# Kernel tuning notes

Hardware: AMD Instinct MI355X
Metric: run time of the kernel (lower is better)

The kernel has to match this reference:

```python
import jax, jax.numpy as jnp
import numpy as np

P = 2
SZ = 224
NIMG = 4
LX, LY, LF, LO = 32, 32, 3, 3
PL, PR, PT, PB = 16, 15, 16, 15
PFO = 1
NFREQ, NORIENT, NPHASE = 12, 8, 2
NFEAT = NPHASE * NORIENT * NFREQ  # 192
CX = SZ + PT + PB - LY + 1  # 224
CY = SZ + PL + PR - LX + 1  # 224


def _gauss(l, w):
    t = np.linspace(-1.0, 1.0, l)
    g = 1.0 / (np.sqrt(2.0 * np.pi) * w) * np.exp(-t ** 2 / (2.0 * w ** 2))
    return g.astype(np.float32)


def _conv2d(x, k):
    # x: [N,1,H,W], k: [1,1,kh,kw]; VALID cross-correlation, matching F.conv2d
    return jax.lax.conv_general_dilated(
        x, k, window_strides=(1, 1), padding='VALID',
        dimension_numbers=('NCHW', 'OIHW', 'NCHW'))


def setup_inputs() -> dict:
    key = jax.random.key(0)
    x = jax.random.normal(key, (NIMG, NFEAT, SZ, SZ), dtype=jnp.float32)
    return {"x": x}


def reference(x):
    gx = jnp.asarray(_gauss(LX, 1.0)).reshape(1, 1, 1, LX)
    gy = jnpy = jnp.asarray(_gauss(LY, 1.0)).reshape(1, 1, LY, 1)
    gf = jnp.asarray(_gauss(LF, 1.0)).reshape(1, 1, LF, 1)
    go = jnp.asarray(_gauss(LO, 1.0)).reshape(1, 1, 1, LO)

    x_p = x ** P
    x_p = jnp.pad(x_p, ((0, 0), (0, 0), (PT, PB), (PL, PR)))  # [B,192,255,255]
    # permute to [feat, img, H, W] then flatten features*imgs into batch
    t = jnp.transpose(x_p, (1, 0, 2, 3)).reshape(NFEAT * NIMG, 1, SZ + PT + PB, SZ + PL + PR)
    t = _conv2d(t, gx)  # [feat*img,1,255,224]
    t = _conv2d(t, gy)  # [feat*img,1,224,224]
    t = t.reshape(NFREQ, NORIENT, NPHASE, NIMG, 1, CX, CY)
    # -> [CX, CY, phase, img, 1, freq, orient]
    t = jnp.transpose(t, (5, 6, 2, 3, 4, 0, 1)).reshape(-1, 1, NFREQ, NORIENT)
    t = jnp.pad(t, ((0, 0), (0, 0), (PFO, PFO), (PFO, PFO)))  # [M,1,14,10]
    t = _conv2d(t, gf)  # [M,1,12,10]
    t = _conv2d(t, go)  # [M,1,12,8]
    B = t.reshape(CX, CY, NPHASE, NIMG, NFREQ, NORIENT)
    return jnp.transpose(B, (3, 4, 5, 2, 0, 1))  # [img,freq,orient,phase,CX,CY]
```

## Files before the change

kernel.cpp:

```cpp
#include <hip/hip_runtime.h>
#include <hip/hip_fp16.h>
#include <math.h>


#define SZW   224
#define PLANE (224*224)
#define PW    256

struct GaussArgs {
    float wx[32];
    float w30;
    float w31;
};

__device__ __forceinline__ int swz(int g) { return g ^ ((g >> 3) & 7); }

__global__ __launch_bounds__(512, 6) void pass1_kernel(const float* __restrict__ in,
                                                       __half* __restrict__ ws,
                                                       const GaussArgs ga)
{
    __shared__ float s2[48 * PW];

    const int tid   = threadIdx.x;
    const int y     = blockIdx.x;
    const int by    = blockIdx.y;
    const int phase = by & 1;
    const int fg    = by >> 1;
    const int img   = blockIdx.z;

    const float w31 = ga.w31;
    const float w30 = ga.w30;

    if (tid < 384) {
        const int lf  = tid >> 6;
        const int xp4 = tid & 63;
        const int f   = 4*fg - 1 + lf;
        const int gsw = swz(xp4);
        float4 a[8];
        if (f >= 0 && f < 12 && xp4 >= 4 && xp4 < 60) {
            const int x0 = xp4*4 - 16;
            const float* base = in + (size_t)(img*192 + f*16 + phase)*PLANE + y*SZW + x0;
            #pragma unroll
            for (int o = 0; o < 8; ++o) {
                float4 v = *reinterpret_cast<const float4*>(base + o*2*PLANE);
                a[o] = make_float4(v.x*v.x, v.y*v.y, v.z*v.z, v.w*v.w);
            }
        } else {
            #pragma unroll
            for (int o = 0; o < 8; ++o) a[o] = make_float4(0.f,0.f,0.f,0.f);
        }
        #pragma unroll
        for (int o = 0; o < 8; ++o) {
            float4 l = (o > 0) ? a[o-1] : make_float4(0.f,0.f,0.f,0.f);
            float4 r = (o < 7) ? a[o+1] : make_float4(0.f,0.f,0.f,0.f);
            float4 b;
            b.x = fmaf(w31, a[o].x, w30*(l.x + r.x));
            b.y = fmaf(w31, a[o].y, w30*(l.y + r.y));
            b.z = fmaf(w31, a[o].z, w30*(l.z + r.z));
            b.w = fmaf(w31, a[o].w, w30*(l.w + r.w));
            *reinterpret_cast<float4*>(&s2[(lf*8 + o)*PW + gsw*4]) = b;
        }
    }
    __syncthreads();

    {
        const int o   = tid >> 6;
        const int xp4 = tid & 63;
        const int gsw = swz(xp4);
        float4 a[6];
        #pragma unroll
        for (int lf = 0; lf < 6; ++lf)
            a[lf] = *reinterpret_cast<const float4*>(&s2[(lf*8 + o)*PW + gsw*4]);
        #pragma unroll
        for (int lf = 1; lf < 5; ++lf) {
            float4 b;
            b.x = fmaf(w31, a[lf].x, w30*(a[lf-1].x + a[lf+1].x));
            b.y = fmaf(w31, a[lf].y, w30*(a[lf-1].y + a[lf+1].y));
            b.z = fmaf(w31, a[lf].z, w30*(a[lf-1].z + a[lf+1].z));
            b.w = fmaf(w31, a[lf].w, w30*(a[lf-1].w + a[lf+1].w));
            *reinterpret_cast<float4*>(&s2[(lf*8 + o)*PW + gsw*4]) = b;
        }
    }
    __syncthreads();

    if (tid < 448) {
        const int r  = tid / 14;
        const int xg = tid - r*14;
        const int lf = 1 + (r >> 3);
        const int o  = r & 7;
        const int fo16 = (4*fg + (r >> 3))*16 + o*2;
        const int x0 = xg * 16;
        const int rowb = (lf*8 + o)*PW;
        const int g0 = 4*xg;

        float acc[16];
        #pragma unroll
        for (int j = 0; j < 16; ++j) acc[j] = 0.f;

        #pragma unroll
        for (int t = 0; t < 12; ++t) {
            const float4 q = *reinterpret_cast<const float4*>(
                &s2[rowb + swz(g0 + t)*4]);
            #pragma unroll
            for (int e = 0; e < 4; ++e) {
                const int m = 4*t + e;
                const float qv = (e==0)?q.x:(e==1)?q.y:(e==2)?q.z:q.w;
                const int jlo = (m - 31 > 0) ? (m - 31) : 0;
                const int jhi = (m < 15) ? m : 15;
                #pragma unroll
                for (int j = jlo; j <= jhi; ++j)
                    acc[j] = fmaf(ga.wx[m - j], qv, acc[j]);
            }
        }

        union { uint4 u4[2]; __half2 h2[8]; } pk;
        #pragma unroll
        for (int s = 0; s < 8; ++s)
            pk.h2[s] = __floats2half2_rn(acc[2*s], acc[2*s+1]);

        __half* op = ws + (size_t)(img*192 + phase)*PLANE + (size_t)y*SZW
                        + (size_t)fo16*PLANE + x0;
        *reinterpret_cast<uint4*>(op)     = pk.u4[0];
        *reinterpret_cast<uint4*>(op + 8) = pk.u4[1];
    }
}

#define P2R 143
__global__ __launch_bounds__(512, 4) void pass2_kernel(const __half* __restrict__ ws,
                                                       float* __restrict__ out,
                                                       const GaussArgs ga)
{
    __shared__ __half tile[P2R * SZW];

    const int tid = threadIdx.x;
    const int ch  = blockIdx.x;
    const int yb  = blockIdx.y * 112;

    const __half* wp = ws + (size_t)ch * PLANE;

    for (int t = tid; t < P2R*28; t += 512) {
        const int r = t / 28;
        const int g = t - r*28;
        const int yy = yb - 16 + r;
        uint4 v = make_uint4(0u, 0u, 0u, 0u);
        if (yy >= 0 && yy < SZW)
            v = *reinterpret_cast<const uint4*>(wp + (size_t)yy * SZW + g*8);
        *reinterpret_cast<uint4*>(&tile[r*SZW + g*8]) = v;
    }
    __syncthreads();

    if (tid < 448) {
        const int cp = tid % 112;
        const int gq = tid / 112;
        const int x0 = cp * 2;

        float* oc = out + (size_t)ch * PLANE + x0;

        #pragma unroll 1
        for (int s = 0; s < 2; ++s) {
            const int cc    = gq*2 + s;
            const int sbase = cc * 14;

            float a0[14], a1[14];
            #pragma unroll
            for (int j = 0; j < 14; ++j) { a0[j] = 0.f; a1[j] = 0.f; }

            #pragma unroll
            for (int i = 0; i < 45; ++i) {
                const __half2 h = *reinterpret_cast<const __half2*>(
                    &tile[(sbase + i)*SZW + x0]);
                const float2 f = __half22float2(h);
                const int jlo = (i - 31 > 0) ? (i - 31) : 0;
                const int jhi = (i < 13) ? i : 13;
                #pragma unroll
                for (int j = jlo; j <= jhi; ++j) {
                    a0[j] = fmaf(ga.wx[i - j], f.x, a0[j]);
                    a1[j] = fmaf(ga.wx[i - j], f.y, a1[j]);
                }
            }

            #pragma unroll
            for (int j = 0; j < 14; ++j)
                *reinterpret_cast<float2*>(
                    oc + (size_t)(yb + cc*14 + j) * SZW) = make_float2(a0[j], a1[j]);
        }
    }
}

extern "C" void kernel_launch(void* const* d_in, const int* in_sizes, int n_in,
                              void* d_out, int out_size, void* d_ws, size_t ws_size,
                              hipStream_t stream)
{
    const float* x  = (const float*)d_in[0];
    float*      out = (float*)d_out;
    __half*     ws  = (__half*)d_ws;

    GaussArgs ga;
    const double c0 = 1.0 / sqrt(2.0 * 3.14159265358979323846);
    for (int k = 0; k < 32; ++k) {
        double t = -1.0 + 2.0 * (double)k / 31.0;
        ga.wx[k] = (float)(c0 * exp(-t * t / 2.0));
    }
    ga.w31 = (float)c0;
    ga.w30 = (float)(c0 * exp(-0.5));

    dim3 g1(SZW, 6, 4);
    pass1_kernel<<<g1, 512, 0, stream>>>(x, ws, ga);
    dim3 g2(768, 2);
    pass2_kernel<<<g2, 512, 0, stream>>>(ws, out, ga);
}
```

Before: 109.7 us.

## Load pass2 tile via direct global-to-LDS DMA and pad pass1 shared rows

Pass2 now fills its shared tile with global_load_lds 16-byte transfers instead of loading through registers and storing to LDS. Rows are clamped, and the out-of-range halo rows are zeroed in a second step after a barrier. The convolution loop is moved into a helper and called twice, which replaces the unroll-1 loop with two fully unrolled chunks. The pass1 shared row pitch changes from 256 to 260 floats to alter the bank mapping. The changes add an extra barrier and zeroing pass, raise register pressure from the unrolled chunks, and depend on the global-to-LDS builtin writing its 16-byte data at the expected per-lane LDS addresses.

After: 105.6 us (median of 3 runs). 3.8% less time.

```diff
diff --git a/kernel.cpp b/kernel.cpp
--- a/kernel.cpp
+++ b/kernel.cpp
@@ -5,7 +5,7 @@
 
 #define SZW   224
 #define PLANE (224*224)
-#define PW    256
+#define PW    260
 
 struct GaussArgs {
     float wx[32];
@@ -125,6 +125,33 @@
     }
 }
 
+__device__ __forceinline__ void p2_chunk(const __half* __restrict__ tile,
+                                         const GaussArgs& ga,
+                                         float* __restrict__ oc,
+                                         int yb, int cc, int x0)
+{
+    const int sbase = cc * 14;
+    float a0[14], a1[14];
+    #pragma unroll
+    for (int j = 0; j < 14; ++j) { a0[j] = 0.f; a1[j] = 0.f; }
+    #pragma unroll
+    for (int i = 0; i < 45; ++i) {
+        const __half2 h = *reinterpret_cast<const __half2*>(&tile[(sbase + i)*SZW + x0]);
+        const float2 f = __half22float2(h);
+        const int jlo = (i - 31 > 0) ? (i - 31) : 0;
+        const int jhi = (i < 13) ? i : 13;
+        #pragma unroll
+        for (int j = jlo; j <= jhi; ++j) {
+            a0[j] = fmaf(ga.wx[i - j], f.x, a0[j]);
+            a1[j] = fmaf(ga.wx[i - j], f.y, a1[j]);
+        }
+    }
+    #pragma unroll
+    for (int j = 0; j < 14; ++j)
+        *reinterpret_cast<float2*>(oc + (size_t)(yb + cc*14 + j) * SZW) =
+            make_float2(a0[j], a1[j]);
+}
+
 #define P2R 143
 __global__ __launch_bounds__(512, 4) void pass2_kernel(const __half* __restrict__ ws,
                                                        float* __restrict__ out,
@@ -141,11 +168,21 @@
     for (int t = tid; t < P2R*28; t += 512) {
         const int r = t / 28;
         const int g = t - r*28;
-        const int yy = yb - 16 + r;
-        uint4 v = make_uint4(0u, 0u, 0u, 0u);
-        if (yy >= 0 && yy < SZW)
-            v = *reinterpret_cast<const uint4*>(wp + (size_t)yy * SZW + g*8);
-        *reinterpret_cast<uint4*>(&tile[r*SZW + g*8]) = v;
+        int yy = yb - 16 + r;
+        yy = (yy < 0) ? 0 : (yy > SZW-1 ? SZW-1 : yy);
+        __builtin_amdgcn_global_load_lds(
+            (const __attribute__((address_space(1))) void*)(wp + (size_t)yy*SZW + g*8),
+            (__attribute__((address_space(3))) void*)(&tile[(size_t)t*8]),
+            16, 0, 0);
+    }
+    __syncthreads();
+
+    if (blockIdx.y == 0) {
+        for (int t = tid; t < 16*28; t += 512)
+            *reinterpret_cast<uint4*>(&tile[(size_t)t*8]) = make_uint4(0u,0u,0u,0u);
+    } else {
+        for (int t = tid; t < 15*28; t += 512)
+            *reinterpret_cast<uint4*>(&tile[(size_t)(128*28 + t)*8]) = make_uint4(0u,0u,0u,0u);
     }
     __syncthreads();
 
@@ -153,37 +190,10 @@
         const int cp = tid % 112;
         const int gq = tid / 112;
         const int x0 = cp * 2;
-
         float* oc = out + (size_t)ch * PLANE + x0;
 
-        #pragma unroll 1
-        for (int s = 0; s < 2; ++s) {
-            const int cc    = gq*2 + s;
-            const int sbase = cc * 14;
-
-            float a0[14], a1[14];
-            #pragma unroll
-            for (int j = 0; j < 14; ++j) { a0[j] = 0.f; a1[j] = 0.f; }
-
-            #pragma unroll
-            for (int i = 0; i < 45; ++i) {
-                const __half2 h = *reinterpret_cast<const __half2*>(
-                    &tile[(sbase + i)*SZW + x0]);
-                const float2 f = __half22float2(h);
-                const int jlo = (i - 31 > 0) ? (i - 31) : 0;
-                const int jhi = (i < 13) ? i : 13;
-                #pragma unroll
-                for (int j = jlo; j <= jhi; ++j) {
-                    a0[j] = fmaf(ga.wx[i - j], f.x, a0[j]);
-                    a1[j] = fmaf(ga.wx[i - j], f.y, a1[j]);
-                }
-            }
-
-            #pragma unroll
-            for (int j = 0; j < 14; ++j)
-                *reinterpret_cast<float2*>(
-                    oc + (size_t)(yb + cc*14 + j) * SZW) = make_float2(a0[j], a1[j]);
-        }
+        p2_chunk(tile, ga, oc, yb, gq*2,     x0);
+        p2_chunk(tile, ga, oc, yb, gq*2 + 1, x0);
     }
 }
 
```
